# Performance work log

Measured on AMD Instinct MI355X. Metric: run time of the kernel, lower is better.

The kernel has to match this reference:

```python
import jax, jax.numpy as jnp
import numpy as np

HEADS = 16
KV_HEADS = 4
DIM_HEAD = 128
DIM = 2048
ROPE_BASE = 10000.0


def rotate_half(t):
    t1, t2 = jnp.split(t, 2, axis=-1)
    return jnp.concatenate((-t2, t1), axis=-1)


def apply_rotary(t, cos, sin):
    # t: [b, h, n, d]; cos/sin: [n, d]
    return t * cos + rotate_half(t) * sin


def setup_inputs() -> dict:
    key = jax.random.key(0)
    ks = jax.random.split(key, 6)
    b, n = 4, 1024
    s = 1.0 / np.sqrt(DIM)
    x = jax.random.normal(ks[0], (b, n, DIM), dtype=jnp.float32)
    Wq = jax.random.normal(ks[1], (DIM, HEADS * DIM_HEAD), dtype=jnp.float32) * s
    Wk = jax.random.normal(ks[2], (DIM, KV_HEADS * DIM_HEAD), dtype=jnp.float32) * s
    Wv = jax.random.normal(ks[3], (DIM, KV_HEADS * DIM_HEAD), dtype=jnp.float32) * s
    Wo = jax.random.normal(ks[4], (HEADS * DIM_HEAD, DIM), dtype=jnp.float32) * s
    head_scale = 1.0 + 0.02 * jax.random.normal(ks[5], (1, HEADS, 1, 1), dtype=jnp.float32)
    return {"x": x, "Wq": Wq, "Wk": Wk, "Wv": Wv, "Wo": Wo, "head_scale": head_scale}


def reference(x, Wq, Wk, Wv, Wo, head_scale):
    b, n, _ = x.shape
    # projections
    q = (x @ Wq).reshape(b, n, HEADS, DIM_HEAD).transpose(0, 2, 1, 3)      # b h n d
    k = (x @ Wk).reshape(b, n, KV_HEADS, DIM_HEAD).transpose(0, 2, 1, 3)   # b kv n d
    v = (x @ Wv).reshape(b, n, KV_HEADS, DIM_HEAD).transpose(0, 2, 1, 3)
    # rotary embeddings
    inv_freq = 1.0 / (ROPE_BASE ** (jnp.arange(0, DIM_HEAD, 2, dtype=jnp.float32) / DIM_HEAD))
    freqs = jnp.arange(n, dtype=jnp.float32)[:, None] * inv_freq[None, :]  # n, d/2
    emb = jnp.concatenate((freqs, freqs), axis=-1)                          # n, d
    cos, sin = jnp.cos(emb), jnp.sin(emb)
    q = apply_rotary(q, cos, sin)
    k = apply_rotary(k, cos, sin)
    # GQA: expand kv heads to query heads
    rep = HEADS // KV_HEADS
    k = jnp.repeat(k, rep, axis=1)
    v = jnp.repeat(v, rep, axis=1)
    # attention with causal mask
    scale = 1.0 / jnp.sqrt(jnp.array(DIM_HEAD, dtype=x.dtype))
    scores = jnp.einsum('bhid,bhjd->bhij', q, k) * scale
    causal = jnp.tril(jnp.ones((n, n), dtype=bool))
    scores = jnp.where(causal, scores, jnp.finfo(scores.dtype).min)
    attn = jax.nn.softmax(scores, axis=-1)
    out = jnp.einsum('bhij,bhjd->bhid', attn, v)
    out = out * head_scale                                                  # learned per-head scale
    out = out.transpose(0, 2, 1, 3).reshape(b, n, HEADS * DIM_HEAD)
    return out @ Wo
```

## Files before the change

### kernel.cpp

```cpp
#include <hip/hip_runtime.h>

typedef __attribute__((ext_vector_type(8))) short short8;
typedef __attribute__((ext_vector_type(8), may_alias)) short short8a;
typedef __attribute__((ext_vector_type(4))) short short4a_ __attribute__((may_alias));
typedef __attribute__((ext_vector_type(2), may_alias)) short short2a;
typedef __attribute__((ext_vector_type(4))) float float4_;
typedef __attribute__((ext_vector_type(4), may_alias)) float float4a;
typedef __attribute__((ext_vector_type(2), may_alias)) float float2a;

__device__ __forceinline__ float b2f(short h) {
  unsigned int u = ((unsigned int)(unsigned short)h) << 16;
  return __builtin_bit_cast(float, u);
}
__device__ __forceinline__ short f2b(float f) {
  unsigned int u = __builtin_bit_cast(unsigned int, f);
  u += 0x7fffu + ((u >> 16) & 1u);
  return (short)(unsigned short)(u >> 16);
}

#define GLOBAL_AS __attribute__((address_space(1)))
#define LDS_AS    __attribute__((address_space(3)))
__device__ __forceinline__ void async_copy16(void* lds, const void* g) {
  __builtin_amdgcn_global_load_lds((GLOBAL_AS const void*)g, (LDS_AS void*)lds, 16, 0, 0);
}

__global__ __launch_bounds__(256) void prep(const float* __restrict__ x,
                                            const float* __restrict__ Wq,
                                            const float* __restrict__ Wk,
                                            const float* __restrict__ Wv,
                                            const float* __restrict__ Wo,
                                            short* __restrict__ xb,
                                            short* __restrict__ wqkvt,
                                            short* __restrict__ wot,
                                            float* __restrict__ rtab) {
  __shared__ float tile[64][65];
  int bid = blockIdx.x;
  if (bid < 1536) {
    int k0 = (bid & 31) * 64, n0 = (bid >> 5) * 64;
    for (int idx = threadIdx.x; idx < 4096; idx += 256) {
      int r = idx >> 6, cc = idx & 63;
      int n = n0 + cc;
      float v;
      if (n < 2048)      v = Wq[(size_t)(k0 + r) * 2048 + n] * 0.08838834764831845f;
      else if (n < 2560) v = Wk[(size_t)(k0 + r) * 512 + (n - 2048)];
      else               v = Wv[(size_t)(k0 + r) * 512 + (n - 2560)];
      tile[r][cc] = v;
    }
    __syncthreads();
    for (int idx = threadIdx.x; idx < 4096; idx += 256) {
      int r = idx >> 6, cc = idx & 63;
      wqkvt[(size_t)(n0 + r) * 2048 + k0 + cc] = f2b(tile[cc][r]);
    }
  } else if (bid < 2560) {
    int t = bid - 1536;
    int k0 = (t & 31) * 64, n0 = (t >> 5) * 64;
    for (int idx = threadIdx.x; idx < 4096; idx += 256) {
      int r = idx >> 6, cc = idx & 63;
      tile[r][cc] = Wo[(size_t)(k0 + r) * 2048 + n0 + cc];
    }
    __syncthreads();
    for (int idx = threadIdx.x; idx < 4096; idx += 256) {
      int r = idx >> 6, cc = idx & 63;
      wot[(size_t)(n0 + r) * 2048 + k0 + cc] = f2b(tile[cc][r]);
    }
  } else if (bid < 10752) {
    int i = (bid - 2560) * 256 + threadIdx.x;
    float4a v = ((const float4a*)x)[i];
    short4a_ o;
    o.x = f2b(v.x); o.y = f2b(v.y); o.z = f2b(v.z); o.w = f2b(v.w);
    ((short4a_*)xb)[i] = o;
  } else {
    int idx = (bid - 10752) * 256 + threadIdx.x;
    int pos = idx >> 6, i = idx & 63;
    float inv = exp2f((float)i * -0.20762050593478f);
    float s, c;
    sincosf((float)pos * inv, &s, &c);
    float2a cs; cs.x = c; cs.y = s;
    ((float2a*)rtab)[idx] = cs;
  }
}

template <int MODE>
__global__ __launch_bounds__(256, 2)
void gemm_bt(const short* __restrict__ A, const short* __restrict__ B,
             void* __restrict__ Cv, const float* __restrict__ rtab,
             short* __restrict__ vt, int M, int N, int K) {
  __shared__ alignas(16) short lsm[MODE == 1 ? 16896 : 16384];
  short* lA = lsm;
  short* lB = lsm + 8192;
  const int tid = threadIdx.x;
  const int wave = tid >> 6, lane = tid & 63;
  const int quad = lane >> 4, l16 = lane & 15;
  const int m0 = blockIdx.x * 128, n0 = blockIdx.y * 128;
  const int wm = (wave >> 1) * 64, wn = (wave & 1) * 64;
  float4_ acc[4][4];
#pragma unroll
  for (int i = 0; i < 4; i++)
#pragma unroll
    for (int j = 0; j < 4; j++) acc[i][j] = (float4_){0.f, 0.f, 0.f, 0.f};
  const int nK = K >> 6;
  const int srow = lane >> 3, slot = lane & 7;
  for (int kt = 0; kt < nK; ++kt) {
    __syncthreads();
#pragma unroll
    for (int cth = 0; cth < 4; ++cth) {
      int rb = wave * 32 + cth * 8;
      int r = rb + srow;
      int c = slot ^ (r & 7);
      async_copy16(&lA[rb * 64], A + (size_t)(m0 + r) * K + kt * 64 + c * 8);
      async_copy16(&lB[rb * 64], B + (size_t)(n0 + r) * K + kt * 64 + c * 8);
    }
    __syncthreads();
#pragma unroll
    for (int kc = 0; kc < 2; ++kc) {
      short8 af[4], bf[4];
      int cch = kc * 4 + quad;
#pragma unroll
      for (int mt = 0; mt < 4; ++mt) {
        int ar = wm + mt * 16 + l16;
        af[mt] = *(const short8a*)&lA[ar * 64 + (cch ^ (ar & 7)) * 8];
      }
#pragma unroll
      for (int nt = 0; nt < 4; ++nt) {
        int br = wn + nt * 16 + l16;
        bf[nt] = *(const short8a*)&lB[br * 64 + (cch ^ (br & 7)) * 8];
      }
#pragma unroll
      for (int mt = 0; mt < 4; ++mt)
#pragma unroll
        for (int nt = 0; nt < 4; ++nt)
          acc[mt][nt] = __builtin_amdgcn_mfma_f32_16x16x32_bf16(af[mt], bf[nt], acc[mt][nt], 0, 0, 0);
    }
  }
  if (MODE == 1) {
    const bool isRope = (n0 < 2560);
    __syncthreads();
    short* lC = lsm;
    const int posBase = m0 & 1023;
    float4a tv[16];
    if (isRope) {
#pragma unroll
      for (int it = 0; it < 16; ++it) {
        int idx = it * 256 + tid;
        int row = idx >> 5, c2 = (idx & 31) * 2;
        tv[it] = *(const float4a*)&rtab[((size_t)(posBase + row) * 64 + c2) * 2];
      }
    }
#pragma unroll
    for (int mt = 0; mt < 4; ++mt)
#pragma unroll
      for (int nt = 0; nt < 4; ++nt)
#pragma unroll
        for (int r = 0; r < 4; r++)
          lC[(wm + mt * 16 + quad * 4 + r) * 132 + wn + nt * 16 + l16] = f2b(acc[mt][nt][r]);
    __syncthreads();
    if (isRope) {
      short* Cb = (short*)Cv;
#pragma unroll
      for (int it = 0; it < 16; ++it) {
        int idx = it * 256 + tid;
        int row = idx >> 5;
        int c2 = (idx & 31) * 2;
        short2a t1 = *(const short2a*)&lC[row * 132 + c2];
        short2a t2 = *(const short2a*)&lC[row * 132 + c2 + 64];
        float t1a = b2f(t1.x), t1b = b2f(t1.y);
        float t2a = b2f(t2.x), t2b = b2f(t2.y);
        float4a t = tv[it];
        short2a o1, o2;
        o1.x = f2b(t1a * t.x - t2a * t.y); o1.y = f2b(t1b * t.z - t2b * t.w);
        o2.x = f2b(t2a * t.x + t1a * t.y); o2.y = f2b(t2b * t.z + t1b * t.w);
        size_t base = (size_t)(m0 + row) * N + n0;
        *(short2a*)&Cb[base + c2] = o1;
        *(short2a*)&Cb[base + c2 + 64] = o2;
      }
    } else {
      const int bkv = (m0 >> 10) * 4 + ((n0 - 2560) >> 7);
#pragma unroll
      for (int it = 0; it < 8; ++it) {
        int idx = it * 256 + tid;
        int d = idx >> 4, jc = idx & 15;
        short8 v;
#pragma unroll
        for (int k = 0; k < 8; ++k) v[k] = lC[(jc * 8 + k) * 132 + d];
        *(short8a*)&vt[((size_t)(bkv * 128 + d)) * 1024 + posBase + jc * 8] = v;
      }
    }
  } else {
#pragma unroll
    for (int mt = 0; mt < 4; ++mt)
#pragma unroll
      for (int nt = 0; nt < 4; ++nt) {
        int row = m0 + wm + mt * 16 + quad * 4;
        int col = n0 + wn + nt * 16 + l16;
        float4_ v = acc[mt][nt];
        float* Cf = (float*)Cv;
#pragma unroll
        for (int r = 0; r < 4; r++) Cf[(size_t)(row + r) * N + col] = v[r];
      }
  }
}

__global__ __launch_bounds__(256, 2)
void flash(const short* __restrict__ qkv, const short* __restrict__ vt,
           const float* __restrict__ head_scale, short* __restrict__ attn) {
  __shared__ alignas(16) short lK[64 * 128];
  __shared__ alignas(16) short lV[128 * 64];
  __shared__ alignas(16) short lP[4][32 * 72];
  const int tid = threadIdx.x, wave = tid >> 6, lane = tid & 63;
  const int quad = lane >> 4, l16 = lane & 15;
  const int bh = blockIdx.x, b = bh >> 4, h = bh & 15, kv = h >> 2;
  const int qt = 7 - blockIdx.y;
  const int base_w = qt * 128 + wave * 32;
  short8 qf[2][4];
#pragma unroll
  for (int g = 0; g < 2; g++) {
    int qrow = base_w + g * 16 + l16;
    const short* qp = qkv + (size_t)(b * 1024 + qrow) * 3072 + h * 128;
#pragma unroll
    for (int kc = 0; kc < 4; kc++) qf[g][kc] = *(const short8a*)(qp + kc * 32 + quad * 8);
  }
  float4_ O[2][8];
#pragma unroll
  for (int g = 0; g < 2; g++)
#pragma unroll
    for (int i = 0; i < 8; i++) O[g][i] = (float4_){0.f, 0.f, 0.f, 0.f};
  float rsacc[2][4] = {{0.f, 0.f, 0.f, 0.f}, {0.f, 0.f, 0.f, 0.f}};
  const size_t kbase = (size_t)(b * 1024) * 3072 + 2048 + kv * 128;
  const size_t vbase = (size_t)((b * 4 + kv) * 128) * 1024;
  const int slot16 = lane & 15, rr4 = lane >> 4;
  const int slot8 = lane & 7, dr8 = lane >> 3;
  const int nkt = 2 * qt + 2;
  for (int kt = 0; kt < nkt; ++kt) {
    __syncthreads();
#pragma unroll
    for (int cc = 0; cc < 4; ++cc) {
      int rb = wave * 16 + cc * 4;
      int r = rb + rr4;
      int c = slot16 ^ (r & 15);
      async_copy16(&lK[rb * 128], qkv + kbase + (size_t)(kt * 64 + r) * 3072 + c * 8);
    }
#pragma unroll
    for (int cc = 0; cc < 4; ++cc) {
      int db = wave * 32 + cc * 8;
      int d = db + dr8;
      int c = slot8 ^ (d & 7);
      async_copy16(&lV[db * 64], vt + vbase + (size_t)d * 1024 + kt * 64 + c * 8);
    }
    __syncthreads();
    if (kt * 64 > base_w + 31) continue;
    float4_ S[2][4];
#pragma unroll
    for (int st = 0; st < 4; ++st) {
      float4_ s0 = (float4_){0.f, 0.f, 0.f, 0.f}, s1 = s0;
      int kr = st * 16 + l16;
#pragma unroll
      for (int kc = 0; kc < 4; ++kc) {
        int c = kc * 4 + quad;
        short8 kf = *(const short8a*)&lK[kr * 128 + (c ^ (kr & 15)) * 8];
        s0 = __builtin_amdgcn_mfma_f32_16x16x32_bf16(qf[0][kc], kf, s0, 0, 0, 0);
        s1 = __builtin_amdgcn_mfma_f32_16x16x32_bf16(qf[1][kc], kf, s1, 0, 0, 0);
      }
      S[0][st] = s0; S[1][st] = s1;
    }
#pragma unroll
    for (int g = 0; g < 2; g++) {
      int gbase = base_w + g * 16;
      if (kt * 64 + 63 > gbase) {
#pragma unroll
        for (int st = 0; st < 4; ++st)
#pragma unroll
          for (int r = 0; r < 4; r++)
            if (kt * 64 + st * 16 + l16 > gbase + quad * 4 + r) S[g][st][r] = -1e30f;
      }
#pragma unroll
      for (int st = 0; st < 4; ++st)
#pragma unroll
        for (int r = 0; r < 4; r++) {
          float pv = __expf(S[g][st][r]);
          rsacc[g][r] += pv;
          lP[wave][(g * 16 + quad * 4 + r) * 72 + st * 16 + l16] = f2b(pv);
        }
    }
    short8 pf[2][2];
#pragma unroll
    for (int g = 0; g < 2; g++)
#pragma unroll
      for (int kc2 = 0; kc2 < 2; kc2++)
        pf[g][kc2] = *(const short8a*)&lP[wave][(g * 16 + l16) * 72 + kc2 * 32 + quad * 8];
#pragma unroll
    for (int dt = 0; dt < 8; ++dt) {
      int d = dt * 16 + l16;
#pragma unroll
      for (int kc2 = 0; kc2 < 2; kc2++) {
        int c = kc2 * 4 + quad;
        short8 vf = *(const short8a*)&lV[d * 64 + (c ^ (d & 7)) * 8];
        O[0][dt] = __builtin_amdgcn_mfma_f32_16x16x32_bf16(pf[0][kc2], vf, O[0][dt], 0, 0, 0);
        O[1][dt] = __builtin_amdgcn_mfma_f32_16x16x32_bf16(pf[1][kc2], vf, O[1][dt], 0, 0, 0);
      }
    }
  }
  float hs = head_scale[h];
#pragma unroll
  for (int g = 0; g < 2; g++) {
    float l_i[4];
#pragma unroll
    for (int r = 0; r < 4; r++) {
      float rs = rsacc[g][r];
#pragma unroll
      for (int off = 8; off; off >>= 1) rs += __shfl_xor(rs, off, 64);
      l_i[r] = rs;
    }
    int qrow = base_w + g * 16 + quad * 4;
#pragma unroll
    for (int dt = 0; dt < 8; ++dt) {
      int col = h * 128 + dt * 16 + l16;
#pragma unroll
      for (int r = 0; r < 4; r++) {
        float o = O[g][dt][r] * (hs / l_i[r]);
        attn[(size_t)(b * 1024 + qrow + r) * 2048 + col] = f2b(o);
      }
    }
  }
}

extern "C" void kernel_launch(void* const* d_in, const int* in_sizes, int n_in,
                              void* d_out, int out_size, void* d_ws, size_t ws_size,
                              hipStream_t stream) {
  const float* x  = (const float*)d_in[0];
  const float* Wq = (const float*)d_in[1];
  const float* Wk = (const float*)d_in[2];
  const float* Wv = (const float*)d_in[3];
  const float* Wo = (const float*)d_in[4];
  const float* hs = (const float*)d_in[5];
  float* out = (float*)d_out;
  char* ws = (char*)d_ws;
  short* xb    = (short*)(ws);
  short* wqkvt = (short*)(ws + 16777216);
  short* wot   = (short*)(ws + 29360128);
  short* qkv   = (short*)(ws + 37748736);
  short* vt    = (short*)(ws + 62914560);
  short* attn  = xb;
  float* rtab  = out + 8257536;

  prep<<<11008, 256, 0, stream>>>(x, Wq, Wk, Wv, Wo, xb, wqkvt, wot, rtab);
  gemm_bt<1><<<dim3(32, 24), 256, 0, stream>>>(xb, wqkvt, (void*)qkv, rtab, vt, 4096, 3072, 2048);
  flash<<<dim3(64, 8), 256, 0, stream>>>(qkv, vt, hs, attn);
  gemm_bt<0><<<dim3(32, 16), 256, 0, stream>>>(attn, wot, (void*)out, nullptr, nullptr, 4096, 2048, 2048);
}
```

Before: 260.9 us.

## Rewrite bf16 GEMM with 256x256 tiles and double-buffered phased LDS pipeline

Both projection GEMMs now use 512-thread blocks that each compute a 256x256 output tile. Global-to-LDS async copies are double-buffered across K-steps and interleaved with MFMA phases, using explicit barriers, vmcnt waits and s_setprio to overlap loads with compute. The RoPE/V-transpose epilogue is reworked to write out the larger tile in two halves. The aim is to raise data reuse and hide load latency. In exchange the grids shrink to 192 and 128 blocks, which can leave many CUs idle, and each block now needs 128KB of LDS.

```diff
diff --git a/kernel.cpp b/kernel.cpp
--- a/kernel.cpp
+++ b/kernel.cpp
@@ -80,120 +80,175 @@
   }
 }
 
+#define FENCE() __builtin_amdgcn_sched_barrier(0)
+#define WAITV(N) asm volatile("s_waitcnt vmcnt(" #N ")" ::: "memory")
+#define WAIT_TAIL(C) do { if (C) WAITV(4); else WAITV(0); } while (0)
+
+#define STAGE_A(TP, TKK, ST)                                                   \
+  do {                                                                         \
+    if ((ST) < nK) {                                                           \
+      short* d_ = &lsm[(TP) * 32768 + (TKK) * 8192 + wave * 512];              \
+      const short* s_ = Asrc + (size_t)(ST) * 64 + (TKK) * 32;                 \
+      async_copy16(d_, s_);                                                    \
+      async_copy16(d_ + 4096, s_ + 128 * (size_t)K);                           \
+    }                                                                          \
+  } while (0)
+#define STAGE_B(TP, TKK, ST)                                                   \
+  do {                                                                         \
+    if ((ST) < nK) {                                                           \
+      short* d_ = &lsm[(TP) * 32768 + 16384 + (TKK) * 8192 + wave * 512];      \
+      const short* s_ = Bsrc + (size_t)(ST) * 64 + (TKK) * 32;                 \
+      async_copy16(d_, s_);                                                    \
+      async_copy16(d_ + 4096, s_ + 128 * (size_t)K);                           \
+    }                                                                          \
+  } while (0)
+
+#define PHASE(P, KK, MH, STAGE_STMT, WAIT_STMT)                                \
+  do {                                                                         \
+    short8 af[4];                                                              \
+    _Pragma("unroll") for (int mt = 0; mt < 4; ++mt)                           \
+        af[mt] = *(const short8a*)&lsm[(P) * 32768 + (KK) * 8192 +             \
+                                       aoff[(MH) * 4 + mt]];                   \
+    if ((MH) == 0) {                                                           \
+      _Pragma("unroll") for (int nt = 0; nt < 4; ++nt)                         \
+          bf[nt] = *(const short8a*)&lsm[(P) * 32768 + 16384 + (KK) * 8192 +   \
+                                         boff[nt]];                            \
+    }                                                                          \
+    STAGE_STMT;                                                                \
+    FENCE();                                                                   \
+    __builtin_amdgcn_s_barrier();                                              \
+    FENCE();                                                                   \
+    __builtin_amdgcn_s_setprio(1);                                             \
+    _Pragma("unroll") for (int mt = 0; mt < 4; ++mt)                           \
+        _Pragma("unroll") for (int nt = 0; nt < 4; ++nt)                       \
+            acc[(MH) * 4 + mt][nt] = __builtin_amdgcn_mfma_f32_16x16x32_bf16(  \
+                af[mt], bf[nt], acc[(MH) * 4 + mt][nt], 0, 0, 0);              \
+    __builtin_amdgcn_s_setprio(0);                                             \
+    FENCE();                                                                   \
+    WAIT_STMT;                                                                 \
+    __builtin_amdgcn_s_barrier();                                              \
+    FENCE();                                                                   \
+  } while (0)
+
 template <int MODE>
-__global__ __launch_bounds__(256, 2)
+__global__ __launch_bounds__(512, 2)
 void gemm_bt(const short* __restrict__ A, const short* __restrict__ B,
              void* __restrict__ Cv, const float* __restrict__ rtab,
              short* __restrict__ vt, int M, int N, int K) {
-  __shared__ alignas(16) short lsm[MODE == 1 ? 16896 : 16384];
-  short* lA = lsm;
-  short* lB = lsm + 8192;
+  __shared__ alignas(16) short lsm[65536];
   const int tid = threadIdx.x;
   const int wave = tid >> 6, lane = tid & 63;
   const int quad = lane >> 4, l16 = lane & 15;
-  const int m0 = blockIdx.x * 128, n0 = blockIdx.y * 128;
-  const int wm = (wave >> 1) * 64, wn = (wave & 1) * 64;
-  float4_ acc[4][4];
-#pragma unroll
-  for (int i = 0; i < 4; i++)
+  const int m0 = blockIdx.x * 256, n0 = blockIdx.y * 256;
+  const int wm = (wave >> 2) * 128, wn = (wave & 3) * 64;
+  const int nK = K >> 6;
+
+  int aoff[8], boff[4];
+#pragma unroll
+  for (int mt = 0; mt < 8; ++mt) {
+    int r = wm + mt * 16 + l16;
+    aoff[mt] = r * 32 + (quad ^ ((r >> 1) & 3)) * 8;
+  }
+#pragma unroll
+  for (int nt = 0; nt < 4; ++nt) {
+    int r = wn + nt * 16 + l16;
+    boff[nt] = r * 32 + (quad ^ ((r >> 1) & 3)) * 8;
+  }
+  const int r0 = tid >> 2;
+  const int qq = (tid & 3) ^ ((r0 >> 1) & 3);
+  const short* Asrc = A + (size_t)(m0 + r0) * K + qq * 8;
+  const short* Bsrc = B + (size_t)(n0 + r0) * K + qq * 8;
+
+  float4_ acc[8][4];
+#pragma unroll
+  for (int i = 0; i < 8; i++)
 #pragma unroll
     for (int j = 0; j < 4; j++) acc[i][j] = (float4_){0.f, 0.f, 0.f, 0.f};
-  const int nK = K >> 6;
-  const int srow = lane >> 3, slot = lane & 7;
-  for (int kt = 0; kt < nK; ++kt) {
-    __syncthreads();
-#pragma unroll
-    for (int cth = 0; cth < 4; ++cth) {
-      int rb = wave * 32 + cth * 8;
-      int r = rb + srow;
-      int c = slot ^ (r & 7);
-      async_copy16(&lA[rb * 64], A + (size_t)(m0 + r) * K + kt * 64 + c * 8);
-      async_copy16(&lB[rb * 64], B + (size_t)(n0 + r) * K + kt * 64 + c * 8);
-    }
-    __syncthreads();
-#pragma unroll
-    for (int kc = 0; kc < 2; ++kc) {
-      short8 af[4], bf[4];
-      int cch = kc * 4 + quad;
-#pragma unroll
-      for (int mt = 0; mt < 4; ++mt) {
-        int ar = wm + mt * 16 + l16;
-        af[mt] = *(const short8a*)&lA[ar * 64 + (cch ^ (ar & 7)) * 8];
-      }
-#pragma unroll
-      for (int nt = 0; nt < 4; ++nt) {
-        int br = wn + nt * 16 + l16;
-        bf[nt] = *(const short8a*)&lB[br * 64 + (cch ^ (br & 7)) * 8];
-      }
-#pragma unroll
-      for (int mt = 0; mt < 4; ++mt)
-#pragma unroll
-        for (int nt = 0; nt < 4; ++nt)
-          acc[mt][nt] = __builtin_amdgcn_mfma_f32_16x16x32_bf16(af[mt], bf[nt], acc[mt][nt], 0, 0, 0);
-    }
-  }
+  short8 bf[4];
+
+  STAGE_A(0, 0, 0); STAGE_B(0, 0, 0); STAGE_A(0, 1, 0); STAGE_B(0, 1, 0);
+  STAGE_A(1, 0, 1); STAGE_B(1, 0, 1);
+  FENCE();
+  if (nK > 1) WAITV(4); else WAITV(0);
+  __builtin_amdgcn_s_barrier();
+  FENCE();
+
+  for (int t = 0; t < nK; t += 2) {
+    PHASE(0, 0, 0, STAGE_A(1, 1, t + 1), );
+    PHASE(0, 0, 1, STAGE_B(1, 1, t + 1), );
+    PHASE(0, 1, 0, STAGE_A(0, 0, t + 2), );
+    PHASE(0, 1, 1, STAGE_B(0, 0, t + 2), WAIT_TAIL(t + 2 < nK));
+    PHASE(1, 0, 0, STAGE_A(0, 1, t + 2), );
+    PHASE(1, 0, 1, STAGE_B(0, 1, t + 2), );
+    PHASE(1, 1, 0, STAGE_A(1, 0, t + 3), );
+    PHASE(1, 1, 1, STAGE_B(1, 0, t + 3), WAIT_TAIL(t + 3 < nK));
+  }
+
   if (MODE == 1) {
     const bool isRope = (n0 < 2560);
-    __syncthreads();
     short* lC = lsm;
     const int posBase = m0 & 1023;
-    float4a tv[16];
-    if (isRope) {
-#pragma unroll
-      for (int it = 0; it < 16; ++it) {
-        int idx = it * 256 + tid;
-        int row = idx >> 5, c2 = (idx & 31) * 2;
-        tv[it] = *(const float4a*)&rtab[((size_t)(posBase + row) * 64 + c2) * 2];
-      }
-    }
-#pragma unroll
-    for (int mt = 0; mt < 4; ++mt)
-#pragma unroll
-      for (int nt = 0; nt < 4; ++nt)
-#pragma unroll
-        for (int r = 0; r < 4; r++)
-          lC[(wm + mt * 16 + quad * 4 + r) * 132 + wn + nt * 16 + l16] = f2b(acc[mt][nt][r]);
-    __syncthreads();
-    if (isRope) {
-      short* Cb = (short*)Cv;
-#pragma unroll
-      for (int it = 0; it < 16; ++it) {
-        int idx = it * 256 + tid;
-        int row = idx >> 5;
-        int c2 = (idx & 31) * 2;
-        short2a t1 = *(const short2a*)&lC[row * 132 + c2];
-        short2a t2 = *(const short2a*)&lC[row * 132 + c2 + 64];
-        float t1a = b2f(t1.x), t1b = b2f(t1.y);
-        float t2a = b2f(t2.x), t2b = b2f(t2.y);
-        float4a t = tv[it];
-        short2a o1, o2;
-        o1.x = f2b(t1a * t.x - t2a * t.y); o1.y = f2b(t1b * t.z - t2b * t.w);
-        o2.x = f2b(t2a * t.x + t1a * t.y); o2.y = f2b(t2b * t.z + t1b * t.w);
-        size_t base = (size_t)(m0 + row) * N + n0;
-        *(short2a*)&Cb[base + c2] = o1;
-        *(short2a*)&Cb[base + c2 + 64] = o2;
-      }
-    } else {
-      const int bkv = (m0 >> 10) * 4 + ((n0 - 2560) >> 7);
-#pragma unroll
-      for (int it = 0; it < 8; ++it) {
-        int idx = it * 256 + tid;
-        int d = idx >> 4, jc = idx & 15;
-        short8 v;
-#pragma unroll
-        for (int k = 0; k < 8; ++k) v[k] = lC[(jc * 8 + k) * 132 + d];
-        *(short8a*)&vt[((size_t)(bkv * 128 + d)) * 1024 + posBase + jc * 8] = v;
+    short* Cb = (short*)Cv;
+#pragma unroll
+    for (int ph = 0; ph < 2; ++ph) {
+      __syncthreads();
+      if ((wave >> 2) == ph) {
+#pragma unroll
+        for (int mt = 0; mt < 8; ++mt)
+#pragma unroll
+          for (int nt = 0; nt < 4; ++nt)
+#pragma unroll
+            for (int r = 0; r < 4; r++)
+              lC[(mt * 16 + quad * 4 + r) * 264 + wn + nt * 16 + l16] = f2b(acc[mt][nt][r]);
+      }
+      __syncthreads();
+      if (isRope) {
+#pragma unroll
+        for (int it = 0; it < 16; ++it) {
+          int idx = it * 512 + tid;
+          int row = idx >> 6;
+          int grow = ph * 128 + row;
+          int head = (idx >> 5) & 1;
+          int c2 = (idx & 31) * 2;
+          int col = head * 128 + c2;
+          float4a t = *(const float4a*)&rtab[((size_t)(posBase + grow) * 64 + c2) * 2];
+          short2a t1 = *(const short2a*)&lC[row * 264 + col];
+          short2a t2 = *(const short2a*)&lC[row * 264 + col + 64];
+          float t1a = b2f(t1.x), t1b = b2f(t1.y);
+          float t2a = b2f(t2.x), t2b = b2f(t2.y);
+          short2a o1, o2;
+          o1.x = f2b(t1a * t.x - t2a * t.y); o1.y = f2b(t1b * t.z - t2b * t.w);
+          o2.x = f2b(t2a * t.x + t1a * t.y); o2.y = f2b(t2b * t.z + t1b * t.w);
+          size_t base = (size_t)(m0 + grow) * N + n0 + col;
+          *(short2a*)&Cb[base] = o1;
+          *(short2a*)&Cb[base + 64] = o2;
+        }
+      } else {
+        const int bkvBase = (m0 >> 10) * 4;
+        const int nrel = n0 - 2560;
+#pragma unroll
+        for (int it = 0; it < 8; ++it) {
+          int idx = it * 512 + tid;
+          int d = idx >> 4;
+          int jc = idx & 15;
+          int gcol = nrel + d;
+          int kvh = gcol >> 7, dd = gcol & 127;
+          short8 v;
+#pragma unroll
+          for (int k = 0; k < 8; ++k) v[k] = lC[(jc * 8 + k) * 264 + d];
+          *(short8a*)&vt[(size_t)((bkvBase + kvh) * 128 + dd) * 1024 + posBase + ph * 128 + jc * 8] = v;
+        }
       }
     }
   } else {
-#pragma unroll
-    for (int mt = 0; mt < 4; ++mt)
+    float* Cf = (float*)Cv;
+#pragma unroll
+    for (int mt = 0; mt < 8; ++mt)
 #pragma unroll
       for (int nt = 0; nt < 4; ++nt) {
         int row = m0 + wm + mt * 16 + quad * 4;
         int col = n0 + wn + nt * 16 + l16;
         float4_ v = acc[mt][nt];
-        float* Cf = (float*)Cv;
 #pragma unroll
         for (int r = 0; r < 4; r++) Cf[(size_t)(row + r) * N + col] = v[r];
       }
@@ -343,7 +398,7 @@
   float* rtab  = out + 8257536;
 
   prep<<<11008, 256, 0, stream>>>(x, Wq, Wk, Wv, Wo, xb, wqkvt, wot, rtab);
-  gemm_bt<1><<<dim3(32, 24), 256, 0, stream>>>(xb, wqkvt, (void*)qkv, rtab, vt, 4096, 3072, 2048);
+  gemm_bt<1><<<dim3(16, 12), 512, 0, stream>>>(xb, wqkvt, (void*)qkv, rtab, vt, 4096, 3072, 2048);
   flash<<<dim3(64, 8), 256, 0, stream>>>(qkv, vt, hs, attn);
-  gemm_bt<0><<<dim3(32, 16), 256, 0, stream>>>(attn, wot, (void*)out, nullptr, nullptr, 4096, 2048, 2048);
-}
+  gemm_bt<0><<<dim3(16, 8), 512, 0, stream>>>(attn, wot, (void*)out, nullptr, nullptr, 4096, 2048, 2048);
+}
```

Result: slower. 285.2 us (+9.3%).

## Rewrite GEMMs with 8-wave double-buffered async-copy pipeline and larger N tiles

Applied to the files above, without the earlier changes.

Replaces the single-buffered 4-wave GEMM with a 512-thread kernel that double-buffers K tiles in LDS. Async global-to-LDS copies for later stages are issued while MFMAs run, using explicit vmcnt waits, s_barrier phases and setprio. Tiles grow to 128x384 for the QKV projection and 128x256 for the output projection, so each block covers three heads and the epilogue loops over them. This is meant to hide load latency and reduce redundant A-tile traffic, at the cost of more LDS, tighter register pressure and more fragile hand scheduling.

```diff
diff --git a/kernel.cpp b/kernel.cpp
--- a/kernel.cpp
+++ b/kernel.cpp
@@ -80,120 +80,217 @@
   }
 }
 
-template <int MODE>
-__global__ __launch_bounds__(256, 2)
+#define FENCE() __builtin_amdgcn_sched_barrier(0)
+
+template <int N_>
+__device__ __forceinline__ void waitv() {
+  if constexpr (N_ == 8)      asm volatile("s_waitcnt vmcnt(8)" ::: "memory");
+  else if constexpr (N_ == 6) asm volatile("s_waitcnt vmcnt(6)" ::: "memory");
+  else if constexpr (N_ == 4) asm volatile("s_waitcnt vmcnt(4)" ::: "memory");
+  else if constexpr (N_ == 3) asm volatile("s_waitcnt vmcnt(3)" ::: "memory");
+  else                        asm volatile("s_waitcnt vmcnt(0)" ::: "memory");
+}
+
+#define STG(P_, KH_, T_, PART_)                                                    \
+  do { if ((T_) < nK) {                                                            \
+    const size_t co_ = (size_t)(T_) * 64 + (KH_) * 32;                             \
+    if ((PART_) == 0) {                                                            \
+      async_copy16(&lsm[(P_) * BUFSZ + (KH_) * 4096 + wave * 512], Asrc + co_);    \
+      async_copy16(&lsm[(P_) * BUFSZ + 8192 + (KH_) * BBUF + wave * 512],          \
+                   Bsrc + co_);                                                    \
+    } else {                                                                       \
+      async_copy16(&lsm[(P_) * BUFSZ + 8192 + (KH_) * BBUF + 4096 + wave * 512],   \
+                   Bsrc + 128 * (size_t)K + co_);                                  \
+      if (BSLAB == 3)                                                              \
+        async_copy16(&lsm[(P_) * BUFSZ + 8192 + (KH_) * BBUF + 8192 + wave * 512], \
+                     Bsrc + 256 * (size_t)K + co_);                                \
+    }                                                                              \
+  } } while (0)
+
+#define WAITG(G_)                                                                  \
+  do { int rem_ = 2 * nK - 2 - (G_);                                               \
+    if (rem_ >= 2) waitv<2 * LPG>();                                               \
+    else if (rem_ == 1) waitv<LPG>();                                              \
+    else waitv<0>(); } while (0)
+
+#define PHASE8(P_, KK_, MH_, STAGE_STMT, ENDW)                                     \
+  {                                                                                \
+    short8 af[2];                                                                  \
+    _Pragma("unroll") for (int mi = 0; mi < 2; ++mi)                               \
+      af[mi] = *(const short8a*)&lsm[(P_) * BUFSZ + (KK_) * 4096 +                 \
+                                     aoff[(MH_) * 2 + mi]];                        \
+    if ((MH_) == 0) {                                                              \
+      _Pragma("unroll") for (int ni = 0; ni < NF; ++ni)                            \
+        bf[ni] = *(const short8a*)&lsm[(P_) * BUFSZ + 8192 + (KK_) * BBUF +        \
+                                       boff[ni]];                                  \
+    }                                                                              \
+    STAGE_STMT;                                                                    \
+    FENCE();                                                                       \
+    __builtin_amdgcn_s_barrier();                                                  \
+    FENCE();                                                                       \
+    __builtin_amdgcn_s_setprio(1);                                                 \
+    _Pragma("unroll") for (int mi = 0; mi < 2; ++mi)                               \
+      _Pragma("unroll") for (int ni = 0; ni < NF; ++ni)                            \
+        acc[(MH_) * 2 + mi][ni] = __builtin_amdgcn_mfma_f32_16x16x32_bf16(         \
+            af[mi], bf[ni], acc[(MH_) * 2 + mi][ni], 0, 0, 0);                     \
+    __builtin_amdgcn_s_setprio(0);                                                 \
+    FENCE();                                                                       \
+    ENDW;                                                                          \
+    __builtin_amdgcn_s_barrier();                                                  \
+    FENCE();                                                                       \
+  }
+
+#define PHASE4(P_, KK_, STAGE0, STAGE1, ENDW)                                      \
+  {                                                                                \
+    short8 af[4];                                                                  \
+    _Pragma("unroll") for (int mi = 0; mi < 4; ++mi)                               \
+      af[mi] = *(const short8a*)&lsm[(P_) * BUFSZ + (KK_) * 4096 + aoff[mi]];      \
+    short8 bf[4];                                                                  \
+    _Pragma("unroll") for (int ni = 0; ni < 4; ++ni)                               \
+      bf[ni] = *(const short8a*)&lsm[(P_) * BUFSZ + 8192 + (KK_) * BBUF +          \
+                                     boff[ni]];                                    \
+    STAGE0; STAGE1;                                                                \
+    FENCE();                                                                       \
+    __builtin_amdgcn_s_barrier();                                                  \
+    FENCE();                                                                       \
+    __builtin_amdgcn_s_setprio(1);                                                 \
+    _Pragma("unroll") for (int mi = 0; mi < 4; ++mi)                               \
+      _Pragma("unroll") for (int ni = 0; ni < 4; ++ni)                             \
+        acc[mi][ni] = __builtin_amdgcn_mfma_f32_16x16x32_bf16(                     \
+            af[mi], bf[ni], acc[mi][ni], 0, 0, 0);                                 \
+    __builtin_amdgcn_s_setprio(0);                                                 \
+    FENCE();                                                                       \
+    ENDW;                                                                          \
+    __builtin_amdgcn_s_barrier();                                                  \
+    FENCE();                                                                       \
+  }
+
+template <int MODE, int BN>
+__global__ __launch_bounds__(512, 2)
 void gemm_bt(const short* __restrict__ A, const short* __restrict__ B,
              void* __restrict__ Cv, const float* __restrict__ rtab,
              short* __restrict__ vt, int M, int N, int K) {
-  __shared__ alignas(16) short lsm[MODE == 1 ? 16896 : 16384];
-  short* lA = lsm;
-  short* lB = lsm + 8192;
+  constexpr int NF = BN / 64;
+  constexpr int BSLAB = BN / 128;
+  constexpr int LPG = 1 + BSLAB;
+  constexpr int BBUF = BSLAB * 4096;
+  constexpr int BUFSZ = 8192 + 2 * BBUF;
+  __shared__ alignas(16) short lsm[2 * BUFSZ];
   const int tid = threadIdx.x;
   const int wave = tid >> 6, lane = tid & 63;
   const int quad = lane >> 4, l16 = lane & 15;
-  const int m0 = blockIdx.x * 128, n0 = blockIdx.y * 128;
-  const int wm = (wave >> 1) * 64, wn = (wave & 1) * 64;
-  float4_ acc[4][4];
+  const int m0 = blockIdx.x * 128, n0 = blockIdx.y * BN;
+  const int wm = (wave >> 2) * 64, wn = (wave & 3) * (BN / 4);
+  const int nK = K >> 6;
+
+  int aoff[4], boff[NF];
+#pragma unroll
+  for (int j = 0; j < 4; ++j) {
+    int r = wm + j * 16 + l16;
+    aoff[j] = r * 32 + (quad ^ ((r >> 1) & 3)) * 8;
+  }
+#pragma unroll
+  for (int ni = 0; ni < NF; ++ni) {
+    int r = wn + ni * 16 + l16;
+    boff[ni] = r * 32 + (quad ^ ((r >> 1) & 3)) * 8;
+  }
+  const int r0 = tid >> 2;
+  const int qq = (tid & 3) ^ ((r0 >> 1) & 3);
+  const short* Asrc = A + (size_t)(m0 + r0) * K + qq * 8;
+  const short* Bsrc = B + (size_t)(n0 + r0) * K + qq * 8;
+
+  float4_ acc[4][NF];
 #pragma unroll
   for (int i = 0; i < 4; i++)
 #pragma unroll
-    for (int j = 0; j < 4; j++) acc[i][j] = (float4_){0.f, 0.f, 0.f, 0.f};
-  const int nK = K >> 6;
-  const int srow = lane >> 3, slot = lane & 7;
-  for (int kt = 0; kt < nK; ++kt) {
-    __syncthreads();
-#pragma unroll
-    for (int cth = 0; cth < 4; ++cth) {
-      int rb = wave * 32 + cth * 8;
-      int r = rb + srow;
-      int c = slot ^ (r & 7);
-      async_copy16(&lA[rb * 64], A + (size_t)(m0 + r) * K + kt * 64 + c * 8);
-      async_copy16(&lB[rb * 64], B + (size_t)(n0 + r) * K + kt * 64 + c * 8);
-    }
-    __syncthreads();
-#pragma unroll
-    for (int kc = 0; kc < 2; ++kc) {
-      short8 af[4], bf[4];
-      int cch = kc * 4 + quad;
-#pragma unroll
-      for (int mt = 0; mt < 4; ++mt) {
-        int ar = wm + mt * 16 + l16;
-        af[mt] = *(const short8a*)&lA[ar * 64 + (cch ^ (ar & 7)) * 8];
-      }
-#pragma unroll
-      for (int nt = 0; nt < 4; ++nt) {
-        int br = wn + nt * 16 + l16;
-        bf[nt] = *(const short8a*)&lB[br * 64 + (cch ^ (br & 7)) * 8];
-      }
-#pragma unroll
-      for (int mt = 0; mt < 4; ++mt)
-#pragma unroll
-        for (int nt = 0; nt < 4; ++nt)
-          acc[mt][nt] = __builtin_amdgcn_mfma_f32_16x16x32_bf16(af[mt], bf[nt], acc[mt][nt], 0, 0, 0);
-    }
-  }
+    for (int j = 0; j < NF; j++) acc[i][j] = (float4_){0.f, 0.f, 0.f, 0.f};
+
+  STG(0, 0, 0, 0); STG(0, 0, 0, 1);
+  STG(0, 1, 0, 0); STG(0, 1, 0, 1);
+  STG(1, 0, 1, 0); STG(1, 0, 1, 1);
+  FENCE();
+  waitv<2 * LPG>();
+  __builtin_amdgcn_s_barrier();
+  FENCE();
+
+  if constexpr (BN == 384) {
+    short8 bf[NF];
+    for (int t = 0; t < nK; t += 2) {
+      PHASE8(0, 0, 0, STG(1, 1, t + 1, 0), );
+      PHASE8(0, 0, 1, STG(1, 1, t + 1, 1), WAITG(2 * t));
+      PHASE8(0, 1, 0, STG(0, 0, t + 2, 0), );
+      PHASE8(0, 1, 1, STG(0, 0, t + 2, 1), WAITG(2 * t + 1));
+      PHASE8(1, 0, 0, STG(0, 1, t + 2, 0), );
+      PHASE8(1, 0, 1, STG(0, 1, t + 2, 1), WAITG(2 * t + 2));
+      PHASE8(1, 1, 0, STG(1, 0, t + 3, 0), );
+      PHASE8(1, 1, 1, STG(1, 0, t + 3, 1), WAITG(2 * t + 3));
+    }
+  } else {
+    for (int t = 0; t < nK; t += 2) {
+      PHASE4(0, 0, STG(1, 1, t + 1, 0), STG(1, 1, t + 1, 1), WAITG(2 * t));
+      PHASE4(0, 1, STG(0, 0, t + 2, 0), STG(0, 0, t + 2, 1), WAITG(2 * t + 1));
+      PHASE4(1, 0, STG(0, 1, t + 2, 0), STG(0, 1, t + 2, 1), WAITG(2 * t + 2));
+      PHASE4(1, 1, STG(1, 0, t + 3, 0), STG(1, 0, t + 3, 1), WAITG(2 * t + 3));
+    }
+  }
+
   if (MODE == 1) {
-    const bool isRope = (n0 < 2560);
-    __syncthreads();
+    constexpr int LCS = BN + 4;
     short* lC = lsm;
     const int posBase = m0 & 1023;
-    float4a tv[16];
-    if (isRope) {
-#pragma unroll
-      for (int it = 0; it < 16; ++it) {
-        int idx = it * 256 + tid;
-        int row = idx >> 5, c2 = (idx & 31) * 2;
-        tv[it] = *(const float4a*)&rtab[((size_t)(posBase + row) * 64 + c2) * 2];
-      }
-    }
+    short* Cb = (short*)Cv;
+    __syncthreads();
 #pragma unroll
     for (int mt = 0; mt < 4; ++mt)
 #pragma unroll
-      for (int nt = 0; nt < 4; ++nt)
+      for (int ni = 0; ni < NF; ++ni)
 #pragma unroll
         for (int r = 0; r < 4; r++)
-          lC[(wm + mt * 16 + quad * 4 + r) * 132 + wn + nt * 16 + l16] = f2b(acc[mt][nt][r]);
-    __syncthreads();
-    if (isRope) {
-      short* Cb = (short*)Cv;
-#pragma unroll
-      for (int it = 0; it < 16; ++it) {
-        int idx = it * 256 + tid;
-        int row = idx >> 5;
-        int c2 = (idx & 31) * 2;
-        short2a t1 = *(const short2a*)&lC[row * 132 + c2];
-        short2a t2 = *(const short2a*)&lC[row * 132 + c2 + 64];
-        float t1a = b2f(t1.x), t1b = b2f(t1.y);
-        float t2a = b2f(t2.x), t2b = b2f(t2.y);
-        float4a t = tv[it];
-        short2a o1, o2;
-        o1.x = f2b(t1a * t.x - t2a * t.y); o1.y = f2b(t1b * t.z - t2b * t.w);
-        o2.x = f2b(t2a * t.x + t1a * t.y); o2.y = f2b(t2b * t.z + t1b * t.w);
-        size_t base = (size_t)(m0 + row) * N + n0;
-        *(short2a*)&Cb[base + c2] = o1;
-        *(short2a*)&Cb[base + c2 + 64] = o2;
-      }
-    } else {
-      const int bkv = (m0 >> 10) * 4 + ((n0 - 2560) >> 7);
-#pragma unroll
-      for (int it = 0; it < 8; ++it) {
-        int idx = it * 256 + tid;
-        int d = idx >> 4, jc = idx & 15;
-        short8 v;
-#pragma unroll
-        for (int k = 0; k < 8; ++k) v[k] = lC[(jc * 8 + k) * 132 + d];
-        *(short8a*)&vt[((size_t)(bkv * 128 + d)) * 1024 + posBase + jc * 8] = v;
+          lC[(wm + mt * 16 + quad * 4 + r) * LCS + wn + ni * 16 + l16] = f2b(acc[mt][ni][r]);
+    __syncthreads();
+    const int hb = n0 >> 7;
+#pragma unroll
+    for (int hh = 0; hh < 3; ++hh) {
+      const int H = hb + hh;
+      if (H < 20) {
+        for (int it = 0; it < 8; ++it) {
+          int idx = it * 512 + tid;
+          int row = idx >> 5;
+          int c2 = (idx & 31) * 2;
+          float4a tt = *(const float4a*)&rtab[((size_t)(posBase + row) * 64 + c2) * 2];
+          short2a t1 = *(const short2a*)&lC[row * LCS + hh * 128 + c2];
+          short2a t2 = *(const short2a*)&lC[row * LCS + hh * 128 + c2 + 64];
+          float t1a = b2f(t1.x), t1b = b2f(t1.y);
+          float t2a = b2f(t2.x), t2b = b2f(t2.y);
+          short2a o1, o2;
+          o1.x = f2b(t1a * tt.x - t2a * tt.y); o1.y = f2b(t1b * tt.z - t2b * tt.w);
+          o2.x = f2b(t2a * tt.x + t1a * tt.y); o2.y = f2b(t2b * tt.z + t1b * tt.w);
+          size_t base = (size_t)(m0 + row) * N + n0 + hh * 128;
+          *(short2a*)&Cb[base + c2] = o1;
+          *(short2a*)&Cb[base + c2 + 64] = o2;
+        }
+      } else {
+        const int hv = H - 20;
+        const int bb = m0 >> 10;
+        for (int it = 0; it < 4; ++it) {
+          int idx = it * 512 + tid;
+          int d = idx >> 4, jc = idx & 15;
+          short8 v;
+#pragma unroll
+          for (int k = 0; k < 8; ++k) v[k] = lC[(jc * 8 + k) * LCS + hh * 128 + d];
+          *(short8a*)&vt[(size_t)((bb * 4 + hv) * 128 + d) * 1024 + posBase + jc * 8] = v;
+        }
       }
     }
   } else {
+    float* Cf = (float*)Cv;
 #pragma unroll
     for (int mt = 0; mt < 4; ++mt)
 #pragma unroll
-      for (int nt = 0; nt < 4; ++nt) {
+      for (int ni = 0; ni < NF; ++ni) {
         int row = m0 + wm + mt * 16 + quad * 4;
-        int col = n0 + wn + nt * 16 + l16;
-        float4_ v = acc[mt][nt];
-        float* Cf = (float*)Cv;
+        int col = n0 + wn + ni * 16 + l16;
+        float4_ v = acc[mt][ni];
 #pragma unroll
         for (int r = 0; r < 4; r++) Cf[(size_t)(row + r) * N + col] = v[r];
       }
@@ -343,7 +440,7 @@
   float* rtab  = out + 8257536;
 
   prep<<<11008, 256, 0, stream>>>(x, Wq, Wk, Wv, Wo, xb, wqkvt, wot, rtab);
-  gemm_bt<1><<<dim3(32, 24), 256, 0, stream>>>(xb, wqkvt, (void*)qkv, rtab, vt, 4096, 3072, 2048);
+  gemm_bt<1, 384><<<dim3(32, 8), 512, 0, stream>>>(xb, wqkvt, (void*)qkv, rtab, vt, 4096, 3072, 2048);
   flash<<<dim3(64, 8), 256, 0, stream>>>(qkv, vt, hs, attn);
-  gemm_bt<0><<<dim3(32, 16), 256, 0, stream>>>(attn, wot, (void*)out, nullptr, nullptr, 4096, 2048, 2048);
-}
+  gemm_bt<0, 256><<<dim3(32, 8), 512, 0, stream>>>(attn, wot, (void*)out, nullptr, nullptr, 4096, 2048, 2048);
+}
```

Result: faster. 250.3 us (-4.1%).

## Add pipelined 128x256 output-projection GEMM with async LDS double buffering

Applied to the files above, without the earlier changes.

Splits the templated GEMM into a dedicated QKV+RoPE kernel and a new output-projection kernel. The new kernel uses 512 threads, a 128x256 tile, and a multi-stage global_load_lds pipeline with explicit vmcnt waits, raw barriers and setprio around the MFMA blocks, so loads overlap with compute. It uses larger LDS (96KB) and more complex synchronization, which can cut occupancy, and the grid shrinks to 256 blocks, which may underfill the device.

```diff
diff --git a/kernel.cpp b/kernel.cpp
--- a/kernel.cpp
+++ b/kernel.cpp
@@ -80,12 +80,11 @@
   }
 }
 
-template <int MODE>
 __global__ __launch_bounds__(256, 2)
-void gemm_bt(const short* __restrict__ A, const short* __restrict__ B,
-             void* __restrict__ Cv, const float* __restrict__ rtab,
-             short* __restrict__ vt, int M, int N, int K) {
-  __shared__ alignas(16) short lsm[MODE == 1 ? 16896 : 16384];
+void gemm_rope(const short* __restrict__ A, const short* __restrict__ B,
+               short* __restrict__ Cb, const float* __restrict__ rtab,
+               short* __restrict__ vt, int M, int N, int K) {
+  __shared__ alignas(16) short lsm[16896];
   short* lA = lsm;
   short* lB = lsm + 8192;
   const int tid = threadIdx.x;
@@ -132,72 +131,170 @@
           acc[mt][nt] = __builtin_amdgcn_mfma_f32_16x16x32_bf16(af[mt], bf[nt], acc[mt][nt], 0, 0, 0);
     }
   }
-  if (MODE == 1) {
-    const bool isRope = (n0 < 2560);
-    __syncthreads();
-    short* lC = lsm;
-    const int posBase = m0 & 1023;
-    float4a tv[16];
-    if (isRope) {
-#pragma unroll
-      for (int it = 0; it < 16; ++it) {
-        int idx = it * 256 + tid;
-        int row = idx >> 5, c2 = (idx & 31) * 2;
-        tv[it] = *(const float4a*)&rtab[((size_t)(posBase + row) * 64 + c2) * 2];
-      }
-    }
-#pragma unroll
-    for (int mt = 0; mt < 4; ++mt)
-#pragma unroll
-      for (int nt = 0; nt < 4; ++nt)
-#pragma unroll
-        for (int r = 0; r < 4; r++)
-          lC[(wm + mt * 16 + quad * 4 + r) * 132 + wn + nt * 16 + l16] = f2b(acc[mt][nt][r]);
-    __syncthreads();
-    if (isRope) {
-      short* Cb = (short*)Cv;
-#pragma unroll
-      for (int it = 0; it < 16; ++it) {
-        int idx = it * 256 + tid;
-        int row = idx >> 5;
-        int c2 = (idx & 31) * 2;
-        short2a t1 = *(const short2a*)&lC[row * 132 + c2];
-        short2a t2 = *(const short2a*)&lC[row * 132 + c2 + 64];
-        float t1a = b2f(t1.x), t1b = b2f(t1.y);
-        float t2a = b2f(t2.x), t2b = b2f(t2.y);
-        float4a t = tv[it];
-        short2a o1, o2;
-        o1.x = f2b(t1a * t.x - t2a * t.y); o1.y = f2b(t1b * t.z - t2b * t.w);
-        o2.x = f2b(t2a * t.x + t1a * t.y); o2.y = f2b(t2b * t.z + t1b * t.w);
-        size_t base = (size_t)(m0 + row) * N + n0;
-        *(short2a*)&Cb[base + c2] = o1;
-        *(short2a*)&Cb[base + c2 + 64] = o2;
-      }
-    } else {
-      const int bkv = (m0 >> 10) * 4 + ((n0 - 2560) >> 7);
-#pragma unroll
-      for (int it = 0; it < 8; ++it) {
-        int idx = it * 256 + tid;
-        int d = idx >> 4, jc = idx & 15;
-        short8 v;
-#pragma unroll
-        for (int k = 0; k < 8; ++k) v[k] = lC[(jc * 8 + k) * 132 + d];
-        *(short8a*)&vt[((size_t)(bkv * 128 + d)) * 1024 + posBase + jc * 8] = v;
-      }
+  const bool isRope = (n0 < 2560);
+  __syncthreads();
+  short* lC = lsm;
+  const int posBase = m0 & 1023;
+  float4a tv[16];
+  if (isRope) {
+#pragma unroll
+    for (int it = 0; it < 16; ++it) {
+      int idx = it * 256 + tid;
+      int row = idx >> 5, c2 = (idx & 31) * 2;
+      tv[it] = *(const float4a*)&rtab[((size_t)(posBase + row) * 64 + c2) * 2];
+    }
+  }
+#pragma unroll
+  for (int mt = 0; mt < 4; ++mt)
+#pragma unroll
+    for (int nt = 0; nt < 4; ++nt)
+#pragma unroll
+      for (int r = 0; r < 4; r++)
+        lC[(wm + mt * 16 + quad * 4 + r) * 132 + wn + nt * 16 + l16] = f2b(acc[mt][nt][r]);
+  __syncthreads();
+  if (isRope) {
+#pragma unroll
+    for (int it = 0; it < 16; ++it) {
+      int idx = it * 256 + tid;
+      int row = idx >> 5;
+      int c2 = (idx & 31) * 2;
+      short2a t1 = *(const short2a*)&lC[row * 132 + c2];
+      short2a t2 = *(const short2a*)&lC[row * 132 + c2 + 64];
+      float t1a = b2f(t1.x), t1b = b2f(t1.y);
+      float t2a = b2f(t2.x), t2b = b2f(t2.y);
+      float4a t = tv[it];
+      short2a o1, o2;
+      o1.x = f2b(t1a * t.x - t2a * t.y); o1.y = f2b(t1b * t.z - t2b * t.w);
+      o2.x = f2b(t2a * t.x + t1a * t.y); o2.y = f2b(t2b * t.z + t1b * t.w);
+      size_t base = (size_t)(m0 + row) * N + n0;
+      *(short2a*)&Cb[base + c2] = o1;
+      *(short2a*)&Cb[base + c2 + 64] = o2;
     }
   } else {
-#pragma unroll
-    for (int mt = 0; mt < 4; ++mt)
-#pragma unroll
-      for (int nt = 0; nt < 4; ++nt) {
-        int row = m0 + wm + mt * 16 + quad * 4;
-        int col = n0 + wn + nt * 16 + l16;
-        float4_ v = acc[mt][nt];
-        float* Cf = (float*)Cv;
-#pragma unroll
-        for (int r = 0; r < 4; r++) Cf[(size_t)(row + r) * N + col] = v[r];
-      }
-  }
+    const int bkv = (m0 >> 10) * 4 + ((n0 - 2560) >> 7);
+#pragma unroll
+    for (int it = 0; it < 8; ++it) {
+      int idx = it * 256 + tid;
+      int d = idx >> 4, jc = idx & 15;
+      short8 v;
+#pragma unroll
+      for (int k = 0; k < 8; ++k) v[k] = lC[(jc * 8 + k) * 132 + d];
+      *(short8a*)&vt[((size_t)(bkv * 128 + d)) * 1024 + posBase + jc * 8] = v;
+    }
+  }
+}
+
+#define FENCE() __builtin_amdgcn_sched_barrier(0)
+
+template <int N_>
+__device__ __forceinline__ void waitv() {
+  if constexpr (N_ == 6)      asm volatile("s_waitcnt vmcnt(6)" ::: "memory");
+  else if constexpr (N_ == 3) asm volatile("s_waitcnt vmcnt(3)" ::: "memory");
+  else                        asm volatile("s_waitcnt vmcnt(0)" ::: "memory");
+}
+
+#define STG2(P_, KH_, T_, PART_)                                                   \
+  do { if ((T_) < nK) {                                                            \
+    const size_t co_ = (size_t)(T_) * 64 + (KH_) * 32;                             \
+    if ((PART_) == 0) {                                                            \
+      async_copy16(&lsm[(P_) * 24576 + (KH_) * 4096 + wave * 512], Asrc + co_);    \
+      async_copy16(&lsm[(P_) * 24576 + 8192 + (KH_) * 8192 + wave * 512],          \
+                   Bsrc + co_);                                                    \
+    } else {                                                                       \
+      async_copy16(&lsm[(P_) * 24576 + 8192 + (KH_) * 8192 + 4096 + wave * 512],   \
+                   Bsrc + 128 * (size_t)K + co_);                                  \
+    }                                                                              \
+  } } while (0)
+
+#define WAITG2(G_)                                                                 \
+  do { int rem_ = 2 * nK - 2 - (G_);                                               \
+    if (rem_ >= 2) waitv<6>();                                                     \
+    else if (rem_ == 1) waitv<3>();                                                \
+    else waitv<0>(); } while (0)
+
+#define PHASED2(P_, KK_, STAGE0, STAGE1, ENDW)                                     \
+  {                                                                                \
+    short8 af[4];                                                                  \
+    _Pragma("unroll") for (int mi = 0; mi < 4; ++mi)                               \
+      af[mi] = *(const short8a*)&lsm[(P_) * 24576 + (KK_) * 4096 + aoff[mi]];      \
+    short8 bf[4];                                                                  \
+    _Pragma("unroll") for (int ni = 0; ni < 4; ++ni)                               \
+      bf[ni] = *(const short8a*)&lsm[(P_) * 24576 + 8192 + (KK_) * 8192 +          \
+                                     boff[ni]];                                    \
+    STAGE0; STAGE1;                                                                \
+    FENCE();                                                                       \
+    __builtin_amdgcn_s_barrier();                                                  \
+    FENCE();                                                                       \
+    __builtin_amdgcn_s_setprio(1);                                                 \
+    _Pragma("unroll") for (int mi = 0; mi < 4; ++mi)                               \
+      _Pragma("unroll") for (int ni = 0; ni < 4; ++ni)                             \
+        acc[mi][ni] = __builtin_amdgcn_mfma_f32_16x16x32_bf16(                     \
+            af[mi], bf[ni], acc[mi][ni], 0, 0, 0);                                 \
+    __builtin_amdgcn_s_setprio(0);                                                 \
+    FENCE();                                                                       \
+    ENDW;                                                                          \
+    __builtin_amdgcn_s_barrier();                                                  \
+    FENCE();                                                                       \
+  }
+
+__global__ __launch_bounds__(512, 2)
+void gemm_out(const short* __restrict__ A, const short* __restrict__ B,
+              float* __restrict__ Cf, int M, int N, int K) {
+  __shared__ alignas(16) short lsm[49152];
+  const int tid = threadIdx.x;
+  const int wave = tid >> 6, lane = tid & 63;
+  const int quad = lane >> 4, l16 = lane & 15;
+  const int m0 = blockIdx.x * 128, n0 = blockIdx.y * 256;
+  const int wm = (wave >> 2) * 64, wn = (wave & 3) * 64;
+  const int nK = K >> 6;
+
+  int aoff[4], boff[4];
+#pragma unroll
+  for (int j = 0; j < 4; ++j) {
+    int r = wm + j * 16 + l16;
+    aoff[j] = r * 32 + (quad ^ ((r >> 1) & 3)) * 8;
+  }
+#pragma unroll
+  for (int ni = 0; ni < 4; ++ni) {
+    int r = wn + ni * 16 + l16;
+    boff[ni] = r * 32 + (quad ^ ((r >> 1) & 3)) * 8;
+  }
+  const int r0 = tid >> 2;
+  const int qq = (tid & 3) ^ ((r0 >> 1) & 3);
+  const short* Asrc = A + (size_t)(m0 + r0) * K + qq * 8;
+  const short* Bsrc = B + (size_t)(n0 + r0) * K + qq * 8;
+
+  float4_ acc[4][4];
+#pragma unroll
+  for (int i = 0; i < 4; i++)
+#pragma unroll
+    for (int j = 0; j < 4; j++) acc[i][j] = (float4_){0.f, 0.f, 0.f, 0.f};
+
+  STG2(0, 0, 0, 0); STG2(0, 0, 0, 1);
+  STG2(0, 1, 0, 0); STG2(0, 1, 0, 1);
+  STG2(1, 0, 1, 0); STG2(1, 0, 1, 1);
+  FENCE();
+  waitv<6>();
+  __builtin_amdgcn_s_barrier();
+  FENCE();
+
+  for (int t = 0; t < nK; t += 2) {
+    PHASED2(0, 0, STG2(1, 1, t + 1, 0), STG2(1, 1, t + 1, 1), WAITG2(2 * t));
+    PHASED2(0, 1, STG2(0, 0, t + 2, 0), STG2(0, 0, t + 2, 1), WAITG2(2 * t + 1));
+    PHASED2(1, 0, STG2(0, 1, t + 2, 0), STG2(0, 1, t + 2, 1), WAITG2(2 * t + 2));
+    PHASED2(1, 1, STG2(1, 0, t + 3, 0), STG2(1, 0, t + 3, 1), WAITG2(2 * t + 3));
+  }
+
+#pragma unroll
+  for (int mt = 0; mt < 4; ++mt)
+#pragma unroll
+    for (int ni = 0; ni < 4; ++ni) {
+      int row = m0 + wm + mt * 16 + quad * 4;
+      int col = n0 + wn + ni * 16 + l16;
+      float4_ v = acc[mt][ni];
+#pragma unroll
+      for (int r = 0; r < 4; r++) Cf[(size_t)(row + r) * N + col] = v[r];
+    }
 }
 
 __global__ __launch_bounds__(256, 2)
@@ -343,7 +440,7 @@
   float* rtab  = out + 8257536;
 
   prep<<<11008, 256, 0, stream>>>(x, Wq, Wk, Wv, Wo, xb, wqkvt, wot, rtab);
-  gemm_bt<1><<<dim3(32, 24), 256, 0, stream>>>(xb, wqkvt, (void*)qkv, rtab, vt, 4096, 3072, 2048);
+  gemm_rope<<<dim3(32, 24), 256, 0, stream>>>(xb, wqkvt, qkv, rtab, vt, 4096, 3072, 2048);
   flash<<<dim3(64, 8), 256, 0, stream>>>(qkv, vt, hs, attn);
-  gemm_bt<0><<<dim3(32, 16), 256, 0, stream>>>(attn, wot, (void*)out, nullptr, nullptr, 4096, 2048, 2048);
-}
+  gemm_out<<<dim3(32, 8), 512, 0, stream>>>(attn, wot, out, 4096, 2048, 2048);
+}
```

Result: faster. 252.0 us (-3.4%).
